# Performance work log

Hardware: AMD Instinct MI355X
Metric: run time of the kernel (lower is better)

## Reference

```python
import jax, jax.numpy as jnp
import numpy as np

D_MODEL = 1024
B, T_Q, T_KV = 4, 2048, 2048


def _linear_params(key, d_in, d_out):
    kw, kb = jax.random.split(key)
    W = jax.random.normal(kw, (d_out, d_in), dtype=jnp.float32) * 0.02
    b = jax.random.normal(kb, (d_out,), dtype=jnp.float32) * 0.02
    return W, b


def setup_inputs() -> dict:
    key = jax.random.key(0)
    ks = jax.random.split(key, 7)
    latent_space = jax.random.normal(ks[0], (B, T_Q, D_MODEL), dtype=jnp.float32)
    input_space = jax.random.normal(ks[1], (B, T_KV, D_MODEL), dtype=jnp.float32)
    Wl, bl = _linear_params(ks[2], D_MODEL, D_MODEL)
    Wu, bu = _linear_params(ks[3], D_MODEL, D_MODEL)
    WA, bA = _linear_params(ks[4], D_MODEL, D_MODEL)  # A_proj: d -> J (J = d)
    WV, bV = _linear_params(ks[5], D_MODEL, D_MODEL)  # V_proj: J -> d
    Wo, bo = _linear_params(ks[6], D_MODEL, D_MODEL)
    return {
        "latent_space": latent_space, "input_space": input_space,
        "Wl": Wl, "bl": bl, "Wu": Wu, "bu": bu,
        "WA": WA, "bA": bA, "WV": WV, "bV": bV,
        "Wo": Wo, "bo": bo,
    }


def reference(latent_space, input_space, Wl, bl, Wu, bu, WA, bA, WV, bV, Wo, bo):
    # emb_0 = l_proj(latent)            [B, T_q, d]
    emb0 = jnp.einsum('bqd,ed->bqe', latent_space, Wl) + bl
    # l = softmax(u_proj(emb_0), -1)^T  [B, d, T_q]
    l = jax.nn.softmax(jnp.einsum('bqd,ed->bqe', emb0, Wu) + bu, axis=-1)
    l = jnp.swapaxes(l, -2, -1)
    # D = A_proj(input)                 [B, T_kv, J]
    Dm = jnp.einsum('bkd,jd->bkj', input_space, WA) + bA
    # A = softmax(V_proj(D), dim=-2)    softmax over T_kv
    A = jax.nn.softmax(jnp.einsum('bkj,dj->bkd', Dm, WV) + bV, axis=-2)
    # w = A @ l                         [B, T_kv, T_q]
    w = jnp.einsum('bkd,bdq->bkq', A, l)
    # o = w @ o_proj(latent)            [B, T_kv, d]
    ov = jnp.einsum('bqd,ed->bqe', latent_space, Wo) + bo
    o = jnp.einsum('bkq,bqd->bkd', w, ov)
    return o
```

## Files before the change

### kernel.cpp

```cpp
#include <hip/hip_runtime.h>
#include <hip/hip_bf16.h>
#include <stdint.h>

typedef __attribute__((ext_vector_type(8))) short bf16x8;
typedef __attribute__((ext_vector_type(4))) float f32x4;
typedef __attribute__((ext_vector_type(4))) unsigned short u16x4;

#define B_  4
#define T_  2048
#define D_  1024
#define BM  128
#define BN  128
#define BK  32

__device__ __forceinline__ float bf2f(ushort u) {
  union { unsigned int i; float f; } v; v.i = ((unsigned int)u) << 16; return v.f;
}
__device__ __forceinline__ ushort f2bf(float f) {
  return (ushort)(__bfloat16_as_ushort(__float2bfloat16(f)));
}
__device__ __forceinline__ void async16(const void* g, void* l) {
  __builtin_amdgcn_global_load_lds(
      (const __attribute__((address_space(1))) void*)g,
      (__attribute__((address_space(3))) void*)l, 16, 0, 0);
}
__device__ __forceinline__ int swz4(int r) { return (r ^ (r >> 2)) & 3; }

__global__ __launch_bounds__(256)
void prep(const float* __restrict__ lat, const float* __restrict__ inp,
          const float* __restrict__ Wl, const float* __restrict__ bl,
          const float* __restrict__ Wu, const float* __restrict__ bu,
          const float* __restrict__ WA, const float* __restrict__ bA,
          const float* __restrict__ WV, const float* __restrict__ bV,
          const float* __restrict__ Wo, const float* __restrict__ bo,
          ushort* __restrict__ xBf, ushort* __restrict__ xBf2,
          ushort* __restrict__ w1, ushort* __restrict__ w2,
          ushort* __restrict__ wCatWo, float* __restrict__ bc, float* __restrict__ bc2)
{
  __shared__ alignas(16) ushort t[64 * 65];
  const long NW = (long)D_ * D_;
  const int bx = blockIdx.x;
  const int tid = threadIdx.x;
  if (bx < 16384) {
    const float* in = bx < 8192 ? lat : inp;
    ushort* out = bx < 8192 ? xBf : xBf2;
    const long i = (long)(bx & 8191) * 256 + tid;
    const float4 v = *(const float4*)(in + i * 4);
    u16x4 o;
    o[0] = f2bf(v.x); o[1] = f2bf(v.y); o[2] = f2bf(v.z); o[3] = f2bf(v.w);
    *(u16x4*)(out + i * 4) = o;
  } else if (bx < 19456) {
    const int seg = (bx - 16384) >> 10;
    const float* in  = seg == 0 ? Wu : (seg == 1 ? WV : Wo);
    ushort* out = seg == 0 ? w1 : (seg == 1 ? w1 + NW : wCatWo);
    const long i = (long)((bx - 16384) & 1023) * 256 + tid;
    const float4 v = *(const float4*)(in + i * 4);
    u16x4 o;
    o[0] = f2bf(v.x); o[1] = f2bf(v.y); o[2] = f2bf(v.z); o[3] = f2bf(v.w);
    *(u16x4*)(out + i * 4) = o;
  } else if (bx < 19968) {
    const int z = (bx - 19456) >> 8;
    const int w = (bx - 19456) & 255;
    const float* in = z ? WA : Wl;
    ushort* out = z ? w2 + NW : w2;
    const int c0 = (w & 15) * 64, r0 = (w >> 4) * 64;
    const int tx = tid & 15, ty = tid >> 4;
#pragma unroll
    for (int i = 0; i < 4; ++i) {
      const int r = ty + i * 16;
      const float4 v = *(const float4*)(in + (long)(r0 + r) * D_ + c0 + tx * 4);
      t[(tx * 4 + 0) * 65 + r] = f2bf(v.x);
      t[(tx * 4 + 1) * 65 + r] = f2bf(v.y);
      t[(tx * 4 + 2) * 65 + r] = f2bf(v.z);
      t[(tx * 4 + 3) * 65 + r] = f2bf(v.w);
    }
    __syncthreads();
#pragma unroll
    for (int i = 0; i < 4; ++i) {
      const int c = ty + i * 16;
      u16x4 v;
#pragma unroll
      for (int j = 0; j < 4; ++j) v[j] = t[c * 65 + tx * 4 + j];
      *(u16x4*)(out + (long)(c0 + c) * D_ + r0 + tx * 4) = v;
    }
  } else {
    const int z = (bx - 19968) >> 8;
    const int w = (bx - 19968) & 255;
    const float* W    = z ? WV : Wu;
    const float* bin  = z ? bA : bl;
    const float* badd = z ? bV : bu;
    float* out        = z ? bc2 : bc;
    const int wv = tid >> 6, lane = tid & 63;
    const int e = w * 4 + wv;
    const float* row = W + (long)e * D_;
    float s = 0.f;
#pragma unroll
    for (int i = 0; i < 16; ++i) s += row[lane + i * 64] * bin[lane + i * 64];
#pragma unroll
    for (int off = 32; off; off >>= 1) s += __shfl_xor(s, off);
    if (lane == 0) out[e] = s + badd[e];
  }
}

template<bool OUT_F32, bool HAS_BIAS, bool EXP_OUT>
__global__ __launch_bounds__(256, 2)
void gemm_nt(const ushort* __restrict__ A, const ushort* __restrict__ B,
             const float* __restrict__ bias, void* __restrict__ C,
             int N, int K, long sA, long sB, long sC)
{
  __shared__ alignas(16) ushort As[BM * BK];
  __shared__ alignas(16) ushort Bs[BN * BK];
  const int tid  = threadIdx.x;
  const int wave = tid >> 6;
  const int lane = tid & 63;
  const int wm   = wave >> 1;
  const int wn   = wave & 1;
  const int bz   = blockIdx.z;
  const int tileN = blockIdx.x * BN;
  const int tileM = blockIdx.y * BM;
  A += (long)bz * sA;
  B += (long)bz * sB;

  const int lrow   = lane >> 2;
  const int lchunk = (lane & 3) ^ swz4(lrow);

  f32x4 acc[4][4];
#pragma unroll
  for (int i = 0; i < 4; ++i)
#pragma unroll
    for (int j = 0; j < 4; ++j) acc[i][j] = (f32x4){0.f, 0.f, 0.f, 0.f};

  const int frow = lane & 15;
  const int kg   = lane >> 4;
  const int coff = ((kg ^ swz4(frow)) << 3);

  for (int kt = 0; kt < K; kt += BK) {
    __syncthreads();
#pragma unroll
    for (int i = 0; i < 2; ++i) {
      const int rg  = wave * 2 + i;
      const int row = rg * 16 + lrow;
      async16(A + (long)(tileM + row) * K + kt + lchunk * 8, (void*)(As + rg * 16 * BK));
      async16(B + (long)(tileN + row) * K + kt + lchunk * 8, (void*)(Bs + rg * 16 * BK));
    }
    __syncthreads();
    bf16x8 af[4], bfr[4];
#pragma unroll
    for (int mi = 0; mi < 4; ++mi)
      af[mi] = *(const bf16x8*)(As + (wm * 64 + mi * 16 + frow) * BK + coff);
#pragma unroll
    for (int ni = 0; ni < 4; ++ni)
      bfr[ni] = *(const bf16x8*)(Bs + (wn * 64 + ni * 16 + frow) * BK + coff);
#pragma unroll
    for (int mi = 0; mi < 4; ++mi)
#pragma unroll
      for (int ni = 0; ni < 4; ++ni)
        acc[mi][ni] = __builtin_amdgcn_mfma_f32_16x16x32_bf16(af[mi], bfr[ni], acc[mi][ni], 0, 0, 0);
  }

  const int rowbase = tileM + wm * 64 + ((lane >> 4) << 2);
  const int colbase = tileN + wn * 64 + (lane & 15);
#pragma unroll
  for (int ni = 0; ni < 4; ++ni) {
    const int col = colbase + ni * 16;
    float bv = 0.f;
    if constexpr (HAS_BIAS) bv = bias[col];
#pragma unroll
    for (int mi = 0; mi < 4; ++mi) {
#pragma unroll
      for (int r = 0; r < 4; ++r) {
        const int row = rowbase + mi * 16 + r;
        float v = acc[mi][ni][r] + bv;
        if constexpr (EXP_OUT) v = __expf(v);
        const long idx = (long)bz * sC + (long)row * N + col;
        if constexpr (OUT_F32) ((float*)C)[idx] = v;
        else ((ushort*)C)[idx] = f2bf(v);
      }
    }
  }
}

__global__ __launch_bounds__(256, 2)
void gemm_nt_dual(const ushort* __restrict__ A, const ushort* __restrict__ B,
                  const float* __restrict__ bias1, const float* __restrict__ bias2,
                  ushort* __restrict__ C1, ushort* __restrict__ C2, int K)
{
  __shared__ alignas(16) ushort As[BM * BK];
  __shared__ alignas(16) ushort Bs[BN * BK];
  const int tid  = threadIdx.x;
  const int wave = tid >> 6;
  const int lane = tid & 63;
  const int wm   = wave >> 1;
  const int wn   = wave & 1;
  const int tileN = blockIdx.x * BN;
  const int tileM = blockIdx.y * BM;
  const bool second = tileN >= D_;
  ushort* C = second ? C2 : C1;
  const float* bias = second ? bias2 : bias1;
  const int colOfs = second ? D_ : 0;

  const int lrow   = lane >> 2;
  const int lchunk = (lane & 3) ^ swz4(lrow);

  f32x4 acc[4][4];
#pragma unroll
  for (int i = 0; i < 4; ++i)
#pragma unroll
    for (int j = 0; j < 4; ++j) acc[i][j] = (f32x4){0.f, 0.f, 0.f, 0.f};

  const int frow = lane & 15;
  const int kg   = lane >> 4;
  const int coff = ((kg ^ swz4(frow)) << 3);

  for (int kt = 0; kt < K; kt += BK) {
    __syncthreads();
#pragma unroll
    for (int i = 0; i < 2; ++i) {
      const int rg  = wave * 2 + i;
      const int row = rg * 16 + lrow;
      async16(A + (long)(tileM + row) * K + kt + lchunk * 8, (void*)(As + rg * 16 * BK));
      async16(B + (long)(tileN + row) * K + kt + lchunk * 8, (void*)(Bs + rg * 16 * BK));
    }
    __syncthreads();
    bf16x8 af[4], bfr[4];
#pragma unroll
    for (int mi = 0; mi < 4; ++mi)
      af[mi] = *(const bf16x8*)(As + (wm * 64 + mi * 16 + frow) * BK + coff);
#pragma unroll
    for (int ni = 0; ni < 4; ++ni)
      bfr[ni] = *(const bf16x8*)(Bs + (wn * 64 + ni * 16 + frow) * BK + coff);
#pragma unroll
    for (int mi = 0; mi < 4; ++mi)
#pragma unroll
      for (int ni = 0; ni < 4; ++ni)
        acc[mi][ni] = __builtin_amdgcn_mfma_f32_16x16x32_bf16(af[mi], bfr[ni], acc[mi][ni], 0, 0, 0);
  }

  const int rowbase = tileM + wm * 64 + ((lane >> 4) << 2);
  const int colbase = tileN - colOfs + wn * 64 + (lane & 15);
#pragma unroll
  for (int ni = 0; ni < 4; ++ni) {
    const int col = colbase + ni * 16;
    const float bv = bias[col];
#pragma unroll
    for (int mi = 0; mi < 4; ++mi) {
#pragma unroll
      for (int r = 0; r < 4; ++r) {
        const int row = rowbase + mi * 16 + r;
        C[(long)row * D_ + col] = f2bf(acc[mi][ni][r] + bv);
      }
    }
  }
}

__global__ __launch_bounds__(256, 2)
void gemm_nt_splitk2(const ushort* __restrict__ A, const ushort* __restrict__ B,
                     ushort* __restrict__ P)
{
  __shared__ alignas(16) ushort As[BM * BK];
  __shared__ alignas(16) ushort Bs[BN * BK];
  const int tid  = threadIdx.x;
  const int wave = tid >> 6;
  const int lane = tid & 63;
  const int wm   = wave >> 1;
  const int wn   = wave & 1;
  const int bz   = blockIdx.z >> 1;
  const int sp   = blockIdx.z & 1;
  const int tileN = blockIdx.x * BN;
  const int tileM = blockIdx.y * BM;
  const int kStart = sp * (T_ / 2);
  const ushort* Ab = A + (long)bz * D_ * T_ + (long)tileM * T_;
  const ushort* Bb = B + (long)bz * D_ * T_ + (long)tileN * T_;

  const int lrow   = lane >> 2;
  const int lchunk = (lane & 3) ^ swz4(lrow);

  f32x4 acc[4][4];
#pragma unroll
  for (int i = 0; i < 4; ++i)
#pragma unroll
    for (int j = 0; j < 4; ++j) acc[i][j] = (f32x4){0.f, 0.f, 0.f, 0.f};

  const int frow = lane & 15;
  const int kg   = lane >> 4;
  const int coff = ((kg ^ swz4(frow)) << 3);

  for (int kt = kStart; kt < kStart + T_ / 2; kt += BK) {
    __syncthreads();
#pragma unroll
    for (int i = 0; i < 2; ++i) {
      const int rg  = wave * 2 + i;
      const int row = rg * 16 + lrow;
      async16(Ab + (long)row * T_ + kt + lchunk * 8, (void*)(As + rg * 16 * BK));
      async16(Bb + (long)row * T_ + kt + lchunk * 8, (void*)(Bs + rg * 16 * BK));
    }
    __syncthreads();
    bf16x8 af[4], bfr[4];
#pragma unroll
    for (int mi = 0; mi < 4; ++mi)
      af[mi] = *(const bf16x8*)(As + (wm * 64 + mi * 16 + frow) * BK + coff);
#pragma unroll
    for (int ni = 0; ni < 4; ++ni)
      bfr[ni] = *(const bf16x8*)(Bs + (wn * 64 + ni * 16 + frow) * BK + coff);
#pragma unroll
    for (int mi = 0; mi < 4; ++mi)
#pragma unroll
      for (int ni = 0; ni < 4; ++ni)
        acc[mi][ni] = __builtin_amdgcn_mfma_f32_16x16x32_bf16(af[mi], bfr[ni], acc[mi][ni], 0, 0, 0);
  }

  ushort* C = P + ((long)sp * B_ + bz) * (long)D_ * D_;
  const int rowbase = tileM + wm * 64 + ((lane >> 4) << 2);
  const int colbase = tileN + wn * 64 + (lane & 15);
#pragma unroll
  for (int ni = 0; ni < 4; ++ni) {
    const int col = colbase + ni * 16;
#pragma unroll
    for (int mi = 0; mi < 4; ++mi) {
#pragma unroll
      for (int r = 0; r < 4; ++r)
        C[(long)(rowbase + mi * 16 + r) * D_ + col] = f2bf(acc[mi][ni][r]);
    }
  }
}

__global__ __launch_bounds__(256)
void reduce2_scale(const ushort* __restrict__ P, const float* __restrict__ cinv,
                   ushort* __restrict__ MT)
{
  const long stride = (long)B_ * D_ * D_;
  const long base = ((long)blockIdx.x * 256 + threadIdx.x) * 8;
  const int b = (int)(base >> 20);
  const int e0 = (int)(base & (D_ - 1));
  bf16x8 p0 = *(const bf16x8*)(P + base);
  bf16x8 p1 = *(const bf16x8*)(P + stride + base);
  const float4 c0 = *(const float4*)(cinv + (long)b * D_ + e0);
  const float4 c1 = *(const float4*)(cinv + (long)b * D_ + e0 + 4);
  const float cc[8] = {c0.x, c0.y, c0.z, c0.w, c1.x, c1.y, c1.z, c1.w};
  bf16x8 o;
#pragma unroll
  for (int j = 0; j < 8; ++j)
    o[j] = (short)f2bf((bf2f((ushort)p0[j]) + bf2f((ushort)p1[j])) * cc[j]);
  *(bf16x8*)(MT + base) = o;
}

__global__ __launch_bounds__(256)
void softmax_row(ushort* __restrict__ S)
{
  const long base = (long)blockIdx.x * D_;
  const int tid = threadIdx.x;
  float e[4], s = 0.f;
#pragma unroll
  for (int i = 0; i < 4; ++i) { e[i] = __expf(bf2f(S[base + i * 256 + tid])); s += e[i]; }
#pragma unroll
  for (int off = 32; off; off >>= 1) s += __shfl_xor(s, off);
  __shared__ float reds[4];
  if ((tid & 63) == 0) reds[tid >> 6] = s;
  __syncthreads();
  s = reds[0] + reds[1] + reds[2] + reds[3];
  const float inv = 1.f / s;
#pragma unroll
  for (int i = 0; i < 4; ++i)
    S[base + i * 256 + tid] = f2bf(e[i] * inv);
}

__global__ __launch_bounds__(256)
void transpose2(const ushort* __restrict__ l, ushort* __restrict__ lT,
                const ushort* __restrict__ ov, ushort* __restrict__ ovT)
{
  __shared__ alignas(16) ushort t[64 * 65];
  const int z = blockIdx.z;
  const int b = z & (B_ - 1);
  const ushort* in = (z < B_ ? l : ov) + (long)b * T_ * D_;
  ushort* out      = (z < B_ ? lT : ovT) + (long)b * (long)D_ * T_;
  const int c0 = blockIdx.x * 64, r0 = blockIdx.y * 64;
  const int tx = threadIdx.x & 15, ty = threadIdx.x >> 4;
#pragma unroll
  for (int i = 0; i < 4; ++i) {
    const int r = ty + i * 16;
    u16x4 v = *(const u16x4*)(in + (long)(r0 + r) * D_ + c0 + tx * 4);
#pragma unroll
    for (int c = 0; c < 4; ++c) t[(tx * 4 + c) * 65 + r] = v[c];
  }
  __syncthreads();
#pragma unroll
  for (int i = 0; i < 4; ++i) {
    const int c = ty + i * 16;
    u16x4 v;
#pragma unroll
    for (int j = 0; j < 4; ++j) v[j] = t[c * 65 + tx * 4 + j];
    *(u16x4*)(out + (long)(c0 + c) * T_ + r0 + tx * 4) = v;
  }
}

__global__ __launch_bounds__(256)
void colsum_part(const ushort* __restrict__ E, float* __restrict__ psum)
{
  const int d = blockIdx.x * 256 + threadIdx.x;
  const int c = blockIdx.y;
  const int b = blockIdx.z;
  const ushort* p = E + ((long)b * T_ + (long)c * 128) * D_ + d;
  float s = 0.f;
#pragma unroll 4
  for (int r = 0; r < 128; ++r) s += bf2f(p[(long)r * D_]);
  psum[((long)b * 16 + c) * D_ + d] = s;
}

__global__ __launch_bounds__(256)
void colsum_comb(const float* __restrict__ psum, float* __restrict__ cinv)
{
  const int d = blockIdx.x * 256 + threadIdx.x;
  const int b = blockIdx.y;
  float s = 0.f;
#pragma unroll
  for (int c = 0; c < 16; ++c) s += psum[((long)b * 16 + c) * D_ + d];
  cinv[(long)b * D_ + d] = 1.f / s;
}

extern "C" void kernel_launch(void* const* d_in, const int* in_sizes, int n_in,
                              void* d_out, int out_size, void* d_ws, size_t ws_size,
                              hipStream_t stream)
{
  (void)in_sizes; (void)n_in; (void)out_size; (void)ws_size;
  const float* lat = (const float*)d_in[0];
  const float* inp = (const float*)d_in[1];
  const float* Wl  = (const float*)d_in[2];
  const float* bl  = (const float*)d_in[3];
  const float* Wu  = (const float*)d_in[4];
  const float* bu  = (const float*)d_in[5];
  const float* WA  = (const float*)d_in[6];
  const float* bA  = (const float*)d_in[7];
  const float* WV  = (const float*)d_in[8];
  const float* bV  = (const float*)d_in[9];
  const float* Wo  = (const float*)d_in[10];
  const float* bo  = (const float*)d_in[11];

  char* w = (char*)d_ws;
  auto carve = [&](size_t bytes) { char* p = w; w += (bytes + 255) & ~(size_t)255; return p; };
  const long NT = (long)B_ * T_ * D_;
  const long NW = (long)D_ * D_;
  ushort* xBf   = (ushort*)carve(NT * 2);
  ushort* xBf2  = (ushort*)carve(NT * 2);
  ushort* bufA  = (ushort*)carve(NT * 2);
  ushort* bufB  = (ushort*)carve(NT * 2);
  ushort* scr   = (ushort*)carve(NT * 2);
  ushort* MT    = (ushort*)carve((long)B_ * NW * 2);
  ushort* wCat  = (ushort*)carve(3 * NW * 2);
  float*  bc    = (float*)carve(D_ * 4);
  float*  bc2   = (float*)carve(D_ * 4);
  float*  psum  = (float*)carve(64 * 1024 * 4);
  float*  cinv  = (float*)carve(8 * 1024 * 4);
  ushort* w1 = scr;
  ushort* w2 = scr + 2 * NW;
  ushort* ovT = scr;
  ushort* part = bufB;

  const dim3 blk(256, 1, 1);

  prep<<<dim3(20480), blk, 0, stream>>>(lat, inp, Wl, bl, Wu, bu, WA, bA, WV, bV, Wo, bo,
                                        xBf, xBf2, w1, w2, wCat + NW, bc, bc2);
  gemm_nt<false, false, false><<<dim3(8, 8, 2), blk, 0, stream>>>(
      w1, w2, nullptr, wCat, D_, D_, NW, NW, 2 * NW);
  gemm_nt_dual<<<dim3(16, 64, 1), blk, 0, stream>>>(xBf, wCat, bc, bo, bufB, bufA, D_);
  softmax_row<<<dim3(B_ * T_), blk, 0, stream>>>(bufB);
  transpose2<<<dim3(16, 32, 2 * B_), blk, 0, stream>>>(bufB, xBf, bufA, ovT);
  gemm_nt_splitk2<<<dim3(8, 8, B_ * 2), blk, 0, stream>>>(ovT, xBf, part);
  gemm_nt<false, true, true><<<dim3(8, 64, 1), blk, 0, stream>>>(
      xBf2, wCat + 2 * NW, bc2, bufA, D_, D_, 0, 0, 0);
  colsum_part<<<dim3(4, 16, B_), blk, 0, stream>>>(bufA, psum);
  colsum_comb<<<dim3(4, B_, 1), blk, 0, stream>>>(psum, cinv);
  reduce2_scale<<<dim3(2048), blk, 0, stream>>>(part, cinv, MT);
  gemm_nt<true, false, false><<<dim3(8, 16, B_), blk, 0, stream>>>(
      bufA, MT, nullptr, d_out, D_, D_,
      (long)T_ * D_, NW, (long)T_ * D_);
}
```

Before: 336.8 us.

## Replace main GEMMs with 512-thread 256-row tiled kernel using 4-stage async pipeline

Introduces a templated gemm8 kernel with 8 waves, 256xNB tiles and a four-buffer LDS pipeline. It prefetches three K-steps ahead with explicit vmcnt waits, splits the MFMA work into two halves interleaved with loads, and raises priority around the math. Workgroup ids are remapped to spread neighbouring tiles across XCDs. It replaces the dual-output, split-K and output GEMMs, aiming to cut load latency stalls and improve data reuse. The costs are higher LDS and register use, and the kernel hardcodes 32 K-iterations (K=1024), which the split-K case meets via half-offsets.

```diff
diff --git a/kernel.cpp b/kernel.cpp
--- a/kernel.cpp
+++ b/kernel.cpp
@@ -180,146 +180,191 @@
   }
 }
 
-__global__ __launch_bounds__(256, 2)
-void gemm_nt_dual(const ushort* __restrict__ A, const ushort* __restrict__ B,
-                  const float* __restrict__ bias1, const float* __restrict__ bias2,
-                  ushort* __restrict__ C1, ushort* __restrict__ C2, int K)
-{
-  __shared__ alignas(16) ushort As[BM * BK];
-  __shared__ alignas(16) ushort Bs[BN * BK];
+template<int NB, int MODE>
+__global__ __launch_bounds__(512, 2)
+void gemm8(const ushort* __restrict__ A, const ushort* __restrict__ Bm,
+           const float* __restrict__ bias1, const float* __restrict__ bias2,
+           void* __restrict__ C1, void* __restrict__ C2,
+           int ldA, int ldB, long sAz, long sBz, long sCz)
+{
+  constexpr int LPT = 2 + NB / 128;
+  constexpr int WN  = NB / 64;
+  constexpr int WM  = 8 / WN;
+  constexpr int MR  = 256 / (16 * WM);
+  constexpr int MW  = 256 / WM;
+  constexpr int MH  = MR / 2;
+
+  __shared__ alignas(16) ushort Ab[4][256 * 32];
+  __shared__ alignas(16) ushort Bb[4][NB * 32];
+
+  const int gx = gridDim.x, gy = gridDim.y;
+  const int nwg = gx * gy * gridDim.z;
+  int fid = (blockIdx.z * gy + blockIdx.y) * gx + blockIdx.x;
+  fid = (fid & 7) * (nwg >> 3) + (fid >> 3);
+  const int bx = fid % gx;
+  const int by = (fid / gx) % gy;
+  const int bz = fid / (gx * gy);
+
+  const int tileM = by * 256, tileN = bx * NB;
+
+  const ushort* Ap = A;
+  const ushort* Bp = Bm;
+  if constexpr (MODE == 2) {
+    Ap += (long)(bz >> 1) * sAz + (long)(bz & 1) * 1024;
+    Bp += (long)(bz >> 1) * sBz + (long)(bz & 1) * 1024;
+  } else {
+    Ap += (long)bz * sAz;
+    Bp += (long)bz * sBz;
+  }
+
   const int tid  = threadIdx.x;
-  const int wave = tid >> 6;
+  const int wid  = tid >> 6;
   const int lane = tid & 63;
-  const int wm   = wave >> 1;
-  const int wn   = wave & 1;
-  const int tileN = blockIdx.x * BN;
-  const int tileM = blockIdx.y * BM;
-  const bool second = tileN >= D_;
-  ushort* C = second ? C2 : C1;
-  const float* bias = second ? bias2 : bias1;
-  const int colOfs = second ? D_ : 0;
-
-  const int lrow   = lane >> 2;
-  const int lchunk = (lane & 3) ^ swz4(lrow);
-
-  f32x4 acc[4][4];
-#pragma unroll
-  for (int i = 0; i < 4; ++i)
+  const int wm   = wid / WN;
+  const int wn   = wid % WN;
+
+  const int srow = tid >> 2;
+  const int scol = (((tid & 3) ^ ((tid >> 3) & 3)) << 3);
+  const ushort* gA0 = Ap + (long)(tileM + srow) * ldA + scol;
+  const ushort* gA1 = Ap + (long)(tileM + 128 + srow) * ldA + scol;
+  const ushort* gB0 = Bp + (long)(tileN + srow) * ldB + scol;
+  const ushort* gB1 = (NB == 256) ? (Bp + (long)(tileN + 128 + srow) * ldB + scol) : gB0;
+  const int wofs = wid << 9;
+
+  const int frow  = lane & 15;
+  const int cofs  = (((lane >> 4) ^ ((lane >> 1) & 3)) << 3);
+  const int abase = wm * MW + frow;
+  const int bbase = wn * 64 + frow;
+
+  f32x4 acc[MR][4];
+#pragma unroll
+  for (int i = 0; i < MR; ++i)
 #pragma unroll
     for (int j = 0; j < 4; ++j) acc[i][j] = (f32x4){0.f, 0.f, 0.f, 0.f};
 
-  const int frow = lane & 15;
-  const int kg   = lane >> 4;
-  const int coff = ((kg ^ swz4(frow)) << 3);
-
-  for (int kt = 0; kt < K; kt += BK) {
-    __syncthreads();
-#pragma unroll
-    for (int i = 0; i < 2; ++i) {
-      const int rg  = wave * 2 + i;
-      const int row = rg * 16 + lrow;
-      async16(A + (long)(tileM + row) * K + kt + lchunk * 8, (void*)(As + rg * 16 * BK));
-      async16(B + (long)(tileN + row) * K + kt + lchunk * 8, (void*)(Bs + rg * 16 * BK));
-    }
-    __syncthreads();
-    bf16x8 af[4], bfr[4];
-#pragma unroll
-    for (int mi = 0; mi < 4; ++mi)
-      af[mi] = *(const bf16x8*)(As + (wm * 64 + mi * 16 + frow) * BK + coff);
+#pragma unroll
+  for (int p = 0; p < 3; ++p) {
+    const int kt = p * 32;
+    async16(gA0 + kt, Ab[p] + wofs);
+    async16(gA1 + kt, Ab[p] + 4096 + wofs);
+    async16(gB0 + kt, Bb[p] + wofs);
+    if constexpr (NB == 256) async16(gB1 + kt, Bb[p] + 4096 + wofs);
+  }
+  if constexpr (LPT == 4) asm volatile("s_waitcnt vmcnt(8)" ::: "memory");
+  else                    asm volatile("s_waitcnt vmcnt(6)" ::: "memory");
+  __builtin_amdgcn_s_barrier();
+
+  for (int t = 0; t < 32; ++t) {
+    const int cur = t & 3;
+    const int nxt = (t + 3) & 3;
+    const int kt3 = (t + 3) * 32;
+    const bool st = (t < 29);
+    const ushort* __restrict__ Ac = Ab[cur];
+    const ushort* __restrict__ Bc = Bb[cur];
+
+    bf16x8 bf[4], af[MH];
 #pragma unroll
     for (int ni = 0; ni < 4; ++ni)
-      bfr[ni] = *(const bf16x8*)(Bs + (wn * 64 + ni * 16 + frow) * BK + coff);
-#pragma unroll
-    for (int mi = 0; mi < 4; ++mi)
+      bf[ni] = *(const bf16x8*)(Bc + (bbase + ni * 16) * 32 + cofs);
+#pragma unroll
+    for (int mi = 0; mi < MH; ++mi)
+      af[mi] = *(const bf16x8*)(Ac + (abase + mi * 16) * 32 + cofs);
+    if (st) {
+      async16(gA0 + kt3, Ab[nxt] + wofs);
+      async16(gB0 + kt3, Bb[nxt] + wofs);
+    }
+    __builtin_amdgcn_s_barrier();
+    __builtin_amdgcn_s_setprio(1);
+#pragma unroll
+    for (int mi = 0; mi < MH; ++mi)
 #pragma unroll
       for (int ni = 0; ni < 4; ++ni)
-        acc[mi][ni] = __builtin_amdgcn_mfma_f32_16x16x32_bf16(af[mi], bfr[ni], acc[mi][ni], 0, 0, 0);
-  }
-
-  const int rowbase = tileM + wm * 64 + ((lane >> 4) << 2);
-  const int colbase = tileN - colOfs + wn * 64 + (lane & 15);
-#pragma unroll
-  for (int ni = 0; ni < 4; ++ni) {
-    const int col = colbase + ni * 16;
-    const float bv = bias[col];
-#pragma unroll
-    for (int mi = 0; mi < 4; ++mi) {
-#pragma unroll
-      for (int r = 0; r < 4; ++r) {
-        const int row = rowbase + mi * 16 + r;
-        C[(long)row * D_ + col] = f2bf(acc[mi][ni][r] + bv);
-      }
-    }
-  }
-}
-
-__global__ __launch_bounds__(256, 2)
-void gemm_nt_splitk2(const ushort* __restrict__ A, const ushort* __restrict__ B,
-                     ushort* __restrict__ P)
-{
-  __shared__ alignas(16) ushort As[BM * BK];
-  __shared__ alignas(16) ushort Bs[BN * BK];
-  const int tid  = threadIdx.x;
-  const int wave = tid >> 6;
-  const int lane = tid & 63;
-  const int wm   = wave >> 1;
-  const int wn   = wave & 1;
-  const int bz   = blockIdx.z >> 1;
-  const int sp   = blockIdx.z & 1;
-  const int tileN = blockIdx.x * BN;
-  const int tileM = blockIdx.y * BM;
-  const int kStart = sp * (T_ / 2);
-  const ushort* Ab = A + (long)bz * D_ * T_ + (long)tileM * T_;
-  const ushort* Bb = B + (long)bz * D_ * T_ + (long)tileN * T_;
-
-  const int lrow   = lane >> 2;
-  const int lchunk = (lane & 3) ^ swz4(lrow);
-
-  f32x4 acc[4][4];
-#pragma unroll
-  for (int i = 0; i < 4; ++i)
-#pragma unroll
-    for (int j = 0; j < 4; ++j) acc[i][j] = (f32x4){0.f, 0.f, 0.f, 0.f};
-
-  const int frow = lane & 15;
-  const int kg   = lane >> 4;
-  const int coff = ((kg ^ swz4(frow)) << 3);
-
-  for (int kt = kStart; kt < kStart + T_ / 2; kt += BK) {
-    __syncthreads();
-#pragma unroll
-    for (int i = 0; i < 2; ++i) {
-      const int rg  = wave * 2 + i;
-      const int row = rg * 16 + lrow;
-      async16(Ab + (long)row * T_ + kt + lchunk * 8, (void*)(As + rg * 16 * BK));
-      async16(Bb + (long)row * T_ + kt + lchunk * 8, (void*)(Bs + rg * 16 * BK));
-    }
-    __syncthreads();
-    bf16x8 af[4], bfr[4];
-#pragma unroll
-    for (int mi = 0; mi < 4; ++mi)
-      af[mi] = *(const bf16x8*)(As + (wm * 64 + mi * 16 + frow) * BK + coff);
-#pragma unroll
-    for (int ni = 0; ni < 4; ++ni)
-      bfr[ni] = *(const bf16x8*)(Bs + (wn * 64 + ni * 16 + frow) * BK + coff);
-#pragma unroll
-    for (int mi = 0; mi < 4; ++mi)
+        acc[mi][ni] = __builtin_amdgcn_mfma_f32_16x16x32_bf16(af[mi], bf[ni], acc[mi][ni], 0, 0, 0);
+    __builtin_amdgcn_s_setprio(0);
+    __builtin_amdgcn_s_barrier();
+
+    bf16x8 ag[MH];
+#pragma unroll
+    for (int mi = 0; mi < MH; ++mi)
+      ag[mi] = *(const bf16x8*)(Ac + (abase + (MH + mi) * 16) * 32 + cofs);
+    if (st) {
+      async16(gA1 + kt3, Ab[nxt] + 4096 + wofs);
+      if constexpr (NB == 256) async16(gB1 + kt3, Bb[nxt] + 4096 + wofs);
+    }
+    __builtin_amdgcn_s_barrier();
+    __builtin_amdgcn_s_setprio(1);
+#pragma unroll
+    for (int mi = 0; mi < MH; ++mi)
 #pragma unroll
       for (int ni = 0; ni < 4; ++ni)
-        acc[mi][ni] = __builtin_amdgcn_mfma_f32_16x16x32_bf16(af[mi], bfr[ni], acc[mi][ni], 0, 0, 0);
-  }
-
-  ushort* C = P + ((long)sp * B_ + bz) * (long)D_ * D_;
-  const int rowbase = tileM + wm * 64 + ((lane >> 4) << 2);
-  const int colbase = tileN + wn * 64 + (lane & 15);
-#pragma unroll
-  for (int ni = 0; ni < 4; ++ni) {
-    const int col = colbase + ni * 16;
-#pragma unroll
-    for (int mi = 0; mi < 4; ++mi) {
-#pragma unroll
-      for (int r = 0; r < 4; ++r)
-        C[(long)(rowbase + mi * 16 + r) * D_ + col] = f2bf(acc[mi][ni][r]);
+        acc[MH + mi][ni] = __builtin_amdgcn_mfma_f32_16x16x32_bf16(ag[mi], bf[ni], acc[MH + mi][ni], 0, 0, 0);
+    __builtin_amdgcn_s_setprio(0);
+    if (t < 29) {
+      if constexpr (LPT == 4) asm volatile("s_waitcnt vmcnt(8)" ::: "memory");
+      else                    asm volatile("s_waitcnt vmcnt(6)" ::: "memory");
+    } else if (t == 29) {
+      if constexpr (LPT == 4) asm volatile("s_waitcnt vmcnt(4)" ::: "memory");
+      else                    asm volatile("s_waitcnt vmcnt(3)" ::: "memory");
+    } else if (t == 30) {
+      asm volatile("s_waitcnt vmcnt(0)" ::: "memory");
+    }
+    __builtin_amdgcn_s_barrier();
+  }
+
+  const int rowbase  = tileM + wm * MW + ((lane >> 4) << 2);
+  const int colbase0 = wn * 64 + (lane & 15);
+
+  if constexpr (MODE == 0) {
+    const bool second = tileN >= 1024;
+    ushort* Cp = (ushort*)(second ? C2 : C1);
+    const float* bb = second ? bias2 : bias1;
+    const int cb = tileN - (second ? 1024 : 0) + colbase0;
+#pragma unroll
+    for (int ni = 0; ni < 4; ++ni) {
+      const int col = cb + ni * 16;
+      const float bv = bb[col];
+#pragma unroll
+      for (int mi = 0; mi < MR; ++mi)
+#pragma unroll
+        for (int r = 0; r < 4; ++r)
+          Cp[(long)(rowbase + mi * 16 + r) * 1024 + col] = f2bf(acc[mi][ni][r] + bv);
+    }
+  } else if constexpr (MODE == 1) {
+    ushort* Cp = (ushort*)C1;
+    const int cb = tileN + colbase0;
+#pragma unroll
+    for (int ni = 0; ni < 4; ++ni) {
+      const int col = cb + ni * 16;
+      const float bv = bias1[col];
+#pragma unroll
+      for (int mi = 0; mi < MR; ++mi)
+#pragma unroll
+        for (int r = 0; r < 4; ++r)
+          Cp[(long)(rowbase + mi * 16 + r) * 1024 + col] = f2bf(__expf(acc[mi][ni][r] + bv));
+    }
+  } else if constexpr (MODE == 2) {
+    ushort* Cp = (ushort*)C1 + ((long)(bz & 1) * B_ + (bz >> 1)) * ((long)D_ * D_);
+    const int cb = tileN + colbase0;
+#pragma unroll
+    for (int ni = 0; ni < 4; ++ni) {
+      const int col = cb + ni * 16;
+#pragma unroll
+      for (int mi = 0; mi < MR; ++mi)
+#pragma unroll
+        for (int r = 0; r < 4; ++r)
+          Cp[(long)(rowbase + mi * 16 + r) * 1024 + col] = f2bf(acc[mi][ni][r]);
+    }
+  } else {
+    float* Cp = (float*)C1 + (long)bz * sCz;
+    const int cb = tileN + colbase0;
+#pragma unroll
+    for (int ni = 0; ni < 4; ++ni) {
+      const int col = cb + ni * 16;
+#pragma unroll
+      for (int mi = 0; mi < MR; ++mi)
+#pragma unroll
+        for (int r = 0; r < 4; ++r)
+          Cp[(long)(rowbase + mi * 16 + r) * 1024 + col] = acc[mi][ni][r];
     }
   }
 }
@@ -456,21 +501,24 @@
   ushort* part = bufB;
 
   const dim3 blk(256, 1, 1);
+  const dim3 blk5(512, 1, 1);
 
   prep<<<dim3(20480), blk, 0, stream>>>(lat, inp, Wl, bl, Wu, bu, WA, bA, WV, bV, Wo, bo,
                                         xBf, xBf2, w1, w2, wCat + NW, bc, bc2);
   gemm_nt<false, false, false><<<dim3(8, 8, 2), blk, 0, stream>>>(
       w1, w2, nullptr, wCat, D_, D_, NW, NW, 2 * NW);
-  gemm_nt_dual<<<dim3(16, 64, 1), blk, 0, stream>>>(xBf, wCat, bc, bo, bufB, bufA, D_);
+  gemm8<256, 0><<<dim3(8, 32, 1), blk5, 0, stream>>>(
+      xBf, wCat, bc, bo, bufB, bufA, D_, D_, 0, 0, 0);
   softmax_row<<<dim3(B_ * T_), blk, 0, stream>>>(bufB);
   transpose2<<<dim3(16, 32, 2 * B_), blk, 0, stream>>>(bufB, xBf, bufA, ovT);
-  gemm_nt_splitk2<<<dim3(8, 8, B_ * 2), blk, 0, stream>>>(ovT, xBf, part);
-  gemm_nt<false, true, true><<<dim3(8, 64, 1), blk, 0, stream>>>(
-      xBf2, wCat + 2 * NW, bc2, bufA, D_, D_, 0, 0, 0);
+  gemm8<128, 2><<<dim3(8, 4, 8), blk5, 0, stream>>>(
+      ovT, xBf, nullptr, nullptr, part, nullptr, T_, T_, (long)D_ * T_, (long)D_ * T_, 0);
+  gemm8<128, 1><<<dim3(8, 32, 1), blk5, 0, stream>>>(
+      xBf2, wCat + 2 * NW, bc2, nullptr, bufA, nullptr, D_, D_, 0, 0, 0);
   colsum_part<<<dim3(4, 16, B_), blk, 0, stream>>>(bufA, psum);
   colsum_comb<<<dim3(4, B_, 1), blk, 0, stream>>>(psum, cinv);
   reduce2_scale<<<dim3(2048), blk, 0, stream>>>(part, cinv, MT);
-  gemm_nt<true, false, false><<<dim3(8, 16, B_), blk, 0, stream>>>(
-      bufA, MT, nullptr, d_out, D_, D_,
+  gemm8<128, 3><<<dim3(8, 8, 4), blk5, 0, stream>>>(
+      bufA, MT, nullptr, nullptr, d_out, nullptr, D_, D_,
       (long)T_ * D_, NW, (long)T_ * D_);
 }
```

Measured after the change: 330.8 us. Within noise of the previous version (-1.8%).
